# Optimization experiments

Hardware: AMD Instinct MI355X
Metric: run time of the kernel (lower is better)

## Reference

```python
import jax, jax.numpy as jnp
import numpy as np
import math

B, L, D, H = 4, 1024, 768, 12
HD = D // H            # 64
MAX_LEN = 1024         # max_sequence_length


def setup_inputs() -> dict:
    key = jax.random.key(0)
    ks = jax.random.split(key, 10)
    s = 0.02
    return {
        "hidden_states": jax.random.normal(ks[0], (B, L, D), dtype=jnp.float32),
        "Wq": jax.random.normal(ks[1], (D, D), dtype=jnp.float32) * s,
        "bq": jnp.zeros((D,), dtype=jnp.float32),
        "Wk": jax.random.normal(ks[2], (D, D), dtype=jnp.float32) * s,
        "bk": jnp.zeros((D,), dtype=jnp.float32),
        "Wv": jax.random.normal(ks[3], (D, D), dtype=jnp.float32) * s,
        "bv": jnp.zeros((D,), dtype=jnp.float32),
        "Wd": jax.random.normal(ks[4], (D, D), dtype=jnp.float32) * s,
        "bd": jnp.zeros((D,), dtype=jnp.float32),
        "dist_emb": jax.random.normal(ks[5], (2 * MAX_LEN - 1, HD), dtype=jnp.float32) * s,
    }


def reference(hidden_states, Wq, bq, Wk, bk, Wv, bv, Wd, bd, dist_emb):
    b, l, d = hidden_states.shape
    h, hd = H, HD

    def split_heads(x):  # [b,l,d] -> [b,h,l,hd]
        return x.reshape(b, l, h, hd).transpose(0, 2, 1, 3)

    q = split_heads(hidden_states @ Wq + bq)
    k = split_heads(hidden_states @ Wk + bk)
    v = split_heads(hidden_states @ Wv + bv)

    # content-content scores
    scores = jnp.einsum('bhld,bhrd->bhlr', q, k)

    # relative position embedding lookup: distance in [-(l-1), l-1] shifted by MAX_LEN-1
    dist = jnp.arange(l)[:, None] - jnp.arange(l)[None, :] + (MAX_LEN - 1)
    pos = dist_emb[dist].astype(q.dtype)  # [l, l, hd]

    rel_q = jnp.einsum('bhld,lrd->bhlr', q, pos)
    rel_k = jnp.einsum('bhrd,lrd->bhlr', k, pos)
    scores = (scores + rel_q + rel_k) / math.sqrt(hd)

    probs = jax.nn.softmax(scores, axis=-1)  # dropout p=0 (eval)
    ctx = jnp.einsum('bhlr,bhrd->bhld', probs, v)
    ctx = ctx.transpose(0, 2, 1, 3).reshape(b, l, d)
    return ctx @ Wd + bd
```

## Files before the change

### kernel.cpp

```cpp
#include <hip/hip_runtime.h>
#include <hip/hip_bf16.h>
#include <math.h>

typedef __bf16 bf16x8 __attribute__((ext_vector_type(8)));
typedef float f32x4 __attribute__((ext_vector_type(4)));

#define AS1 __attribute__((address_space(1)))
#define AS3 __attribute__((address_space(3)))
typedef AS1 const void gvoid;
typedef AS3 void svoid;

namespace {
constexpr int Bc = 4, Lc = 1024, Dc = 768, Hc = 12, HDc = 64;
constexpr int NKT = 24;
}

static __device__ __forceinline__ ushort f2bf(float f) {
    __hip_bfloat16 h = __float2bfloat16(f);
    return *reinterpret_cast<ushort*>(&h);
}
static __device__ __forceinline__ float bf2f(ushort u) {
    __hip_bfloat16 h;
    *reinterpret_cast<ushort*>(&h) = u;
    return __bfloat162float(h);
}

static __device__ __forceinline__ int sw_us(int row, int col) {
    int line = row >> 1;
    int slot = (((row & 1) << 2) + (col >> 3)) ^ (line & 7);
    return line * 64 + slot * 8 + (col & 7);
}

static __device__ __forceinline__ int o64(int row, int col) {
    return (row << 6) + ((((col >> 3) ^ (row & 7))) << 3) + (col & 7);
}

__global__ void cvt_bf16_k(const float* __restrict__ in, ushort* __restrict__ out,
                           int n, int ntot) {
    int i = blockIdx.x * 256 + threadIdx.x;
    if (i < ntot) out[i] = (i < n) ? f2bf(in[i]) : (ushort)0;
}

__global__ __launch_bounds__(256) void prep_hs(const float* __restrict__ hs,
                                               ushort* __restrict__ oh) {
    int i = blockIdx.x * 256 + threadIdx.x;
    int m = i / 96, c8 = i % 96;
    const float* src = hs + (size_t)m * Dc + c8 * 8;
    float4 x0 = *(const float4*)src;
    float4 x1 = *(const float4*)(src + 4);
    float xs[8] = {x0.x, x0.y, x0.z, x0.w, x1.x, x1.y, x1.z, x1.w};
    ushort hi[8];
#pragma unroll
    for (int j = 0; j < 8; ++j) hi[j] = f2bf(xs[j]);
    int col = c8 * 8, kt = col >> 5, kc = col & 31;
    int mt = m >> 7, row = m & 127;
    int off = (mt * NKT + kt) * 4096 + sw_us(row, kc);
    *(uint4*)(oh + off) = *(uint4*)hi;
}

__global__ __launch_bounds__(256) void prep_w(
    const float* __restrict__ Wq, const float* __restrict__ Wk,
    const float* __restrict__ Wv, const float* __restrict__ Wd,
    ushort* __restrict__ qkvh,
    ushort* __restrict__ wdh, ushort* __restrict__ wdl) {
    int i = blockIdx.x * 256 + threadIdx.x;
    int k = i / 384, n8 = i % 384;
    int which = n8 / 96, nl = (n8 % 96) * 8;
    const float* W = which == 0 ? Wq : which == 1 ? Wk : which == 2 ? Wv : Wd;
    const float* src = W + (size_t)k * Dc + nl;
    float4 x0 = *(const float4*)src;
    float4 x1 = *(const float4*)(src + 4);
    float xs[8] = {x0.x, x0.y, x0.z, x0.w, x1.x, x1.y, x1.z, x1.w};
    int kt = k >> 5, kc = k & 31;
    ushort* dh = (which < 3) ? qkvh : wdh;
    int ngbase = (which < 3) ? which * Dc + nl : nl;
#pragma unroll
    for (int j = 0; j < 8; ++j) {
        float x = xs[j];
        ushort hi = f2bf(x);
        int ng = ngbase + j;
        int nt = ng >> 7, row = ng & 127;
        int off = (nt * NKT + kt) * 4096 + sw_us(row, kc);
        dh[off] = hi;
        if (which == 3) wdl[off] = f2bf(x - bf2f(hi));
    }
}

__global__ __launch_bounds__(256) void gemm_qkv(
    const ushort* __restrict__ Ah, const ushort* __restrict__ Bh,
    const float* __restrict__ b0, const float* __restrict__ b1,
    const float* __restrict__ b2,
    ushort* __restrict__ o0, ushort* __restrict__ o1, ushort* __restrict__ o2) {
    __shared__ uint4 lds4[2][512];

    const int nt = blockIdx.x, mt = blockIdx.y;
    const int tid = threadIdx.x, w = tid >> 6, lane = tid & 63;
    const int wr = w >> 1, wc = w & 1, r = lane & 15, g = lane >> 4;

    const ushort* gsrc = ((w < 2) ? Ah + (size_t)mt * NKT * 4096
                                  : Bh + (size_t)nt * NKT * 4096) + (w & 1) * 2048;
    ushort* ldst = (ushort*)&lds4[w >> 1][0] + (w & 1) * 2048;

    f32x4 acc[4][4];
#pragma unroll
    for (int a = 0; a < 4; ++a)
#pragma unroll
        for (int b = 0; b < 4; ++b) acc[a][b] = (f32x4){0.f, 0.f, 0.f, 0.f};

    for (int kt = 0; kt < NKT; ++kt) {
        __syncthreads();
        const ushort* s = gsrc + kt * 4096 + lane * 8;
#pragma unroll
        for (int c = 0; c < 4; ++c)
            __builtin_amdgcn_global_load_lds((gvoid*)(s + c * 512),
                                             (svoid*)(ldst + c * 512), 16, 0, 0);
        __syncthreads();

        bf16x8 af[4];
#pragma unroll
        for (int mf = 0; mf < 4; ++mf)
            af[mf] = *(const bf16x8*)((const ushort*)&lds4[0][0] +
                                      sw_us(wr * 64 + mf * 16 + r, g * 8));
#pragma unroll
        for (int nf = 0; nf < 4; ++nf) {
            bf16x8 bf = *(const bf16x8*)((const ushort*)&lds4[1][0] +
                                         sw_us(wc * 64 + nf * 16 + r, g * 8));
#pragma unroll
            for (int mf = 0; mf < 4; ++mf)
                acc[mf][nf] = __builtin_amdgcn_mfma_f32_16x16x32_bf16(af[mf], bf, acc[mf][nf], 0, 0, 0);
        }
    }

    const int which = nt / 6;
    const float* bias = which == 0 ? b0 : which == 1 ? b1 : b2;
    ushort* outp = which == 0 ? o0 : which == 1 ? o1 : o2;
    const int nbase = nt * 128 - which * Dc + wc * 64;
    if (which < 2) {
#pragma unroll
        for (int nf = 0; nf < 4; ++nf) {
            int nl = nbase + nf * 16 + r;
            float bb = bias[nl];
            int h = nl >> 6, d = nl & 63;
#pragma unroll
            for (int mf = 0; mf < 4; ++mf) {
                int mbase = mt * 128 + wr * 64 + mf * 16 + g * 4;
#pragma unroll
                for (int i = 0; i < 4; ++i) {
                    int m = mbase + i, bI = m >> 10, l = m & 1023;
                    outp[(((size_t)bI * Hc + h) * Lc + l) * HDc + d] =
                        f2bf(acc[mf][nf][i] + bb);
                }
            }
        }
    } else {
#pragma unroll
        for (int nf = 0; nf < 4; ++nf) {
            int nl = nbase + nf * 16 + r;
            float bb = bias[nl];
            int h = nl >> 6, d = nl & 63;
#pragma unroll
            for (int mf = 0; mf < 4; ++mf) {
                int mbase = mt * 128 + wr * 64 + mf * 16 + g * 4;
                int bI = mbase >> 10, l = mbase & 1023;
                ushort4 c;
                c.x = f2bf(acc[mf][nf][0] + bb);
                c.y = f2bf(acc[mf][nf][1] + bb);
                c.z = f2bf(acc[mf][nf][2] + bb);
                c.w = f2bf(acc[mf][nf][3] + bb);
                *(ushort4*)&outp[((size_t)(bI * Hc + h) * HDc + d) * Lc + l] = c;
            }
        }
    }
}

__global__ __launch_bounds__(256) void gemm_split(
    const ushort* __restrict__ Ah, const ushort* __restrict__ Al,
    const ushort* __restrict__ Bh, const ushort* __restrict__ Bl,
    const float* __restrict__ b0,
    float* __restrict__ of) {
    __shared__ uint4 lds4[4][512];

    const int nt = blockIdx.x, mt = blockIdx.y;
    const int tid = threadIdx.x, w = tid >> 6, lane = tid & 63;
    const int wr = w >> 1, wc = w & 1, r = lane & 15, g = lane >> 4;

    const ushort* gsrc;
    if (w == 0)      gsrc = Ah + (size_t)mt * NKT * 4096;
    else if (w == 1) gsrc = Al + (size_t)mt * NKT * 4096;
    else if (w == 2) gsrc = Bh + (size_t)nt * NKT * 4096;
    else             gsrc = Bl + (size_t)nt * NKT * 4096;
    ushort* ldst = (ushort*)&lds4[w][0];

    f32x4 acc[4][4];
#pragma unroll
    for (int a = 0; a < 4; ++a)
#pragma unroll
        for (int b = 0; b < 4; ++b) acc[a][b] = (f32x4){0.f, 0.f, 0.f, 0.f};

    for (int kt = 0; kt < NKT; ++kt) {
        __syncthreads();
        const ushort* s = gsrc + kt * 4096 + lane * 8;
#pragma unroll
        for (int c = 0; c < 8; ++c)
            __builtin_amdgcn_global_load_lds((gvoid*)(s + c * 512),
                                             (svoid*)(ldst + c * 512), 16, 0, 0);
        __syncthreads();

        bf16x8 af[4][2];
#pragma unroll
        for (int mf = 0; mf < 4; ++mf) {
            int off = sw_us(wr * 64 + mf * 16 + r, g * 8);
            af[mf][0] = *(const bf16x8*)((const ushort*)&lds4[0][0] + off);
            af[mf][1] = *(const bf16x8*)((const ushort*)&lds4[1][0] + off);
        }
#pragma unroll
        for (int nf = 0; nf < 4; ++nf) {
            int off = sw_us(wc * 64 + nf * 16 + r, g * 8);
            bf16x8 bh = *(const bf16x8*)((const ushort*)&lds4[2][0] + off);
            bf16x8 bl = *(const bf16x8*)((const ushort*)&lds4[3][0] + off);
#pragma unroll
            for (int mf = 0; mf < 4; ++mf) {
                acc[mf][nf] = __builtin_amdgcn_mfma_f32_16x16x32_bf16(af[mf][0], bh, acc[mf][nf], 0, 0, 0);
                acc[mf][nf] = __builtin_amdgcn_mfma_f32_16x16x32_bf16(af[mf][0], bl, acc[mf][nf], 0, 0, 0);
                acc[mf][nf] = __builtin_amdgcn_mfma_f32_16x16x32_bf16(af[mf][1], bh, acc[mf][nf], 0, 0, 0);
            }
        }
    }

#pragma unroll
    for (int nf = 0; nf < 4; ++nf) {
        int n = nt * 128 + wc * 64 + nf * 16 + r;
        float bb = b0[n];
#pragma unroll
        for (int mf = 0; mf < 4; ++mf) {
            int mbase = mt * 128 + wr * 64 + mf * 16 + g * 4;
#pragma unroll
            for (int i = 0; i < 4; ++i) {
                int m = mbase + i;
                of[(size_t)m * Dc + n] = acc[mf][nf][i] + bb;
            }
        }
    }
}

__global__ __launch_bounds__(256, 3) void attn_mfma(
    const ushort* __restrict__ qg, const ushort* __restrict__ kg,
    const ushort* __restrict__ vtg, const ushort* __restrict__ Eb,
    ushort* __restrict__ ctxh, ushort* __restrict__ ctxl)
{
    const int b = blockIdx.z, h = blockIdx.y;
    const int l0 = blockIdx.x * 64;
    const size_t bh = (size_t)(b * Hc + h) * Lc * HDc;
    const ushort* qh = qg + bh;
    const ushort* kh = kg + bh;
    const ushort* vth = vtg + bh;

    __shared__ ushort sK[64 * 64];
    __shared__ ushort sVt[64 * 64];
    __shared__ ushort sE[128 * 64];
    __shared__ ushort sQE[64 * 70];
    __shared__ ushort sKE[64 * 70];

    const int tid = threadIdx.x;
    const int lane = tid & 63;
    const int w = tid >> 6;
    const int g = lane >> 4;
    const int r = lane & 15;

    bf16x8 qf0, qf1;
    {
        const ushort* qrow = qh + (size_t)(l0 + 16 * w + r) * 64;
        qf0 = *reinterpret_cast<const bf16x8*>(qrow + g * 8);
        qf1 = *reinterpret_cast<const bf16x8*>(qrow + 32 + g * 8);
    }

    f32x4 cacc[4];
#pragma unroll
    for (int cf = 0; cf < 4; ++cf) cacc[cf] = (f32x4){0.f, 0.f, 0.f, 0.f};
    float mrun[4], lrun[4];
#pragma unroll
    for (int i = 0; i < 4; ++i) { mrun[i] = -1e30f; lrun[i] = 0.f; }

    for (int r0 = 0; r0 < Lc; r0 += 64) {
        __syncthreads();
#pragma unroll
        for (int i = 0; i < 2; ++i) {
            int idx = tid + i * 256;
            int row = idx >> 3, seg = idx & 7;
            int d = (row << 6) + ((seg ^ (row & 7)) << 3);
            *reinterpret_cast<uint4*>(&sK[d]) =
                *reinterpret_cast<const uint4*>(kh + (size_t)(r0 + row) * 64 + seg * 8);
            *reinterpret_cast<uint4*>(&sVt[d]) =
                *reinterpret_cast<const uint4*>(vth + (size_t)row * Lc + r0 + seg * 8);
        }
        const int jb = l0 - r0 + 960;
#pragma unroll
        for (int c = tid; c < 1024; c += 256) {
            int row = c >> 3, seg = c & 7;
            uint4 val;
            if (row < 127)
                val = *reinterpret_cast<const uint4*>(Eb + (size_t)(jb + row) * 64 + seg * 8);
            else
                val = make_uint4(0, 0, 0, 0);
            *reinterpret_cast<uint4*>(&sE[(row << 6) + ((seg ^ (row & 7)) << 3)]) = val;
        }
        __syncthreads();

        __builtin_amdgcn_s_setprio(1);
        f32x4 S[4];
#pragma unroll
        for (int cf = 0; cf < 4; ++cf) {
            f32x4 acc = (f32x4){0.f, 0.f, 0.f, 0.f};
            bf16x8 kf0 = *reinterpret_cast<const bf16x8*>(&sK[o64(16 * cf + r, g * 8)]);
            bf16x8 kf1 = *reinterpret_cast<const bf16x8*>(&sK[o64(16 * cf + r, 32 + g * 8)]);
            acc = __builtin_amdgcn_mfma_f32_16x16x32_bf16(qf0, kf0, acc, 0, 0, 0);
            acc = __builtin_amdgcn_mfma_f32_16x16x32_bf16(qf1, kf1, acc, 0, 0, 0);
            S[cf] = acc;
        }
        bf16x8 kaf0 = *reinterpret_cast<const bf16x8*>(&sK[o64(16 * w + r, g * 8)]);
        bf16x8 kaf1 = *reinterpret_cast<const bf16x8*>(&sK[o64(16 * w + r, 32 + g * 8)]);
#pragma unroll
        for (int cc = 0; cc < 5; ++cc) {
            {
                int er = 16 * (w + cc) + r;
                bf16x8 e0 = *reinterpret_cast<const bf16x8*>(&sE[o64(er, g * 8)]);
                bf16x8 e1 = *reinterpret_cast<const bf16x8*>(&sE[o64(er, 32 + g * 8)]);
                f32x4 aq = (f32x4){0.f, 0.f, 0.f, 0.f};
                aq = __builtin_amdgcn_mfma_f32_16x16x32_bf16(qf0, e0, aq, 0, 0, 0);
                aq = __builtin_amdgcn_mfma_f32_16x16x32_bf16(qf1, e1, aq, 0, 0, 0);
#pragma unroll
                for (int i = 0; i < 4; ++i) {
                    int lc = 16 * cc + r - 4 * g - i;
                    if ((unsigned)lc < 64u)
                        sQE[(16 * w + 4 * g + i) * 70 + lc] = f2bf(aq[i]);
                }
            }
            {
                int er = 16 * (3 - w + cc) + r;
                bf16x8 e0 = *reinterpret_cast<const bf16x8*>(&sE[o64(er, g * 8)]);
                bf16x8 e1 = *reinterpret_cast<const bf16x8*>(&sE[o64(er, 32 + g * 8)]);
                f32x4 ak = (f32x4){0.f, 0.f, 0.f, 0.f};
                ak = __builtin_amdgcn_mfma_f32_16x16x32_bf16(kaf0, e0, ak, 0, 0, 0);
                ak = __builtin_amdgcn_mfma_f32_16x16x32_bf16(kaf1, e1, ak, 0, 0, 0);
#pragma unroll
                for (int i = 0; i < 4; ++i) {
                    int lc = 16 * cc + r + 4 * g + i - 15;
                    if ((unsigned)lc < 64u)
                        sKE[(16 * w + 4 * g + i) * 70 + lc] = f2bf(ak[i]);
                }
            }
        }
        __builtin_amdgcn_s_setprio(0);
        __syncthreads();

        float p[4][4];
#pragma unroll
        for (int cf = 0; cf < 4; ++cf) {
#pragma unroll
            for (int i = 0; i < 4; ++i) {
                int qr = 16 * w + 4 * g + i;
                int kc = 16 * cf + r;
                p[cf][i] = (S[cf][i] + bf2f(sQE[qr * 70 + 63 - kc])
                                     + bf2f(sKE[kc * 70 + qr])) * 0.125f;
            }
        }
#pragma unroll
        for (int i = 0; i < 4; ++i) {
            float m0 = fmaxf(fmaxf(p[0][i], p[1][i]), fmaxf(p[2][i], p[3][i]));
#pragma unroll
            for (int off = 1; off < 16; off <<= 1) m0 = fmaxf(m0, __shfl_xor(m0, off));
            float mn = fmaxf(mrun[i], m0);
            float sc = __expf(mrun[i] - mn);
            mrun[i] = mn;
            float rsum = 0.f;
#pragma unroll
            for (int cf = 0; cf < 4; ++cf) {
                float e = __expf(p[cf][i] - mn);
                p[cf][i] = e;
                rsum += e;
            }
#pragma unroll
            for (int off = 1; off < 16; off <<= 1) rsum += __shfl_xor(rsum, off);
            lrun[i] = lrun[i] * sc + rsum;
#pragma unroll
            for (int cf = 0; cf < 4; ++cf) cacc[cf][i] *= sc;
        }
#pragma unroll
        for (int cf = 0; cf < 4; ++cf)
#pragma unroll
            for (int i = 0; i < 4; ++i)
                sE[o64(16 * w + 4 * g + i, 16 * cf + r)] = f2bf(p[cf][i]);
        __syncthreads();

        __builtin_amdgcn_s_setprio(1);
        bf16x8 pf0 = *reinterpret_cast<const bf16x8*>(&sE[o64(16 * w + r, g * 8)]);
        bf16x8 pf1 = *reinterpret_cast<const bf16x8*>(&sE[o64(16 * w + r, 32 + g * 8)]);
#pragma unroll
        for (int cf = 0; cf < 4; ++cf) {
            bf16x8 vf0 = *reinterpret_cast<const bf16x8*>(&sVt[o64(16 * cf + r, g * 8)]);
            bf16x8 vf1 = *reinterpret_cast<const bf16x8*>(&sVt[o64(16 * cf + r, 32 + g * 8)]);
            cacc[cf] = __builtin_amdgcn_mfma_f32_16x16x32_bf16(pf0, vf0, cacc[cf], 0, 0, 0);
            cacc[cf] = __builtin_amdgcn_mfma_f32_16x16x32_bf16(pf1, vf1, cacc[cf], 0, 0, 0);
        }
        __builtin_amdgcn_s_setprio(0);
    }

    float rinv[4];
#pragma unroll
    for (int i = 0; i < 4; ++i) rinv[i] = 1.0f / lrun[i];
#pragma unroll
    for (int cf = 0; cf < 4; ++cf) {
#pragma unroll
        for (int i = 0; i < 4; ++i) {
            int qr = 16 * w + 4 * g + i;
            float val = cacc[cf][i] * rinv[i];
            ushort hi = f2bf(val);
            ushort lo = f2bf(val - bf2f(hi));
            int m = b * Lc + l0 + qr;
            int c = h * HDc + 16 * cf + r;
            int off = ((m >> 7) * NKT + (c >> 5)) * 4096 + sw_us(m & 127, c & 31);
            ctxh[off] = hi;
            ctxl[off] = lo;
        }
    }
}

extern "C" void kernel_launch(void* const* d_in, const int* in_sizes, int n_in,
                              void* d_out, int out_size, void* d_ws, size_t ws_size,
                              hipStream_t stream) {
    const float* hs = (const float*)d_in[0];
    const float* Wq = (const float*)d_in[1];
    const float* bq = (const float*)d_in[2];
    const float* Wk = (const float*)d_in[3];
    const float* bk = (const float*)d_in[4];
    const float* Wv = (const float*)d_in[5];
    const float* bv = (const float*)d_in[6];
    const float* Wd = (const float*)d_in[7];
    const float* bd = (const float*)d_in[8];
    const float* Eg = (const float*)d_in[9];

    const size_t N = (size_t)Bc * Lc * Dc;
    ushort* p = (ushort*)d_ws;
    ushort* qbf   = p;               p += N;
    ushort* kbf   = p;               p += N;
    ushort* vbf   = p;               p += N;
    ushort* hsh   = p;               p += N;
    ushort* hsl   = p;               p += N;
    ushort* wqkvh = p;               p += (size_t)2304 * 768;
    ushort* Ebf   = p;               p += (size_t)2048 * HDc;
    ushort* wdh   = p;               p += (size_t)768 * 768;
    ushort* wdl   = p;               p += (size_t)768 * 768;

    const int NE = (2 * 1024 - 1) * HDc;
    const int NEP = 2048 * HDc;

    cvt_bf16_k<<<dim3(512), dim3(256), 0, stream>>>(Eg, Ebf, NE, NEP);
    prep_hs<<<dim3(1536), dim3(256), 0, stream>>>(hs, hsh);
    prep_w<<<dim3(1152), dim3(256), 0, stream>>>(Wq, Wk, Wv, Wd, wqkvh, wdh, wdl);

    gemm_qkv<<<dim3(18, 32), dim3(256), 0, stream>>>(
        hsh, wqkvh, bq, bk, bv, qbf, kbf, vbf);

    attn_mfma<<<dim3(16, Hc, Bc), dim3(256), 0, stream>>>(
        qbf, kbf, vbf, Ebf, hsh, hsl);

    gemm_split<<<dim3(6, 32), dim3(256), 0, stream>>>(
        hsh, hsl, wdh, wdl, bd, (float*)d_out);
}
```

Before: 251.3 us.

## Prefetch attention tiles into registers and halve output GEMM N-tile

The attention loop now issues global loads for the next K, V^T and distance-embedding tiles into registers before computing the current tile, overlapping memory latency with MFMA work. It also removes a barrier after writing probabilities to shared memory, relying on each wave touching only its own rows. The output projection GEMM uses 64-wide N tiles, doubling the block count to improve occupancy across CUs. In exchange, the attention kernel needs more registers, and the missing barrier is a correctness risk.

```diff
diff --git a/kernel.cpp b/kernel.cpp
--- a/kernel.cpp
+++ b/kernel.cpp
@@ -178,46 +178,56 @@
     const ushort* __restrict__ Bh, const ushort* __restrict__ Bl,
     const float* __restrict__ b0,
     float* __restrict__ of) {
-    __shared__ uint4 lds4[4][512];
-
-    const int nt = blockIdx.x, mt = blockIdx.y;
+    __shared__ ushort sA[2][4096];
+    __shared__ ushort sB[2][2048];
+
+    const int nt = blockIdx.x;
+    const int mt = blockIdx.y;
     const int tid = threadIdx.x, w = tid >> 6, lane = tid & 63;
     const int wr = w >> 1, wc = w & 1, r = lane & 15, g = lane >> 4;
-
-    const ushort* gsrc;
-    if (w == 0)      gsrc = Ah + (size_t)mt * NKT * 4096;
-    else if (w == 1) gsrc = Al + (size_t)mt * NKT * 4096;
-    else if (w == 2) gsrc = Bh + (size_t)nt * NKT * 4096;
-    else             gsrc = Bl + (size_t)nt * NKT * 4096;
-    ushort* ldst = (ushort*)&lds4[w][0];
-
-    f32x4 acc[4][4];
+    const int nt2 = nt >> 1, nhalf = nt & 1;
+
+    const ushort* srcs[6];
+    ushort* dsts[6];
+#pragma unroll
+    for (int j = 0; j < 6; ++j) {
+        int c = 6 * w + j;
+        if (c < 8)       { srcs[j] = Ah + (size_t)mt * NKT * 4096 + c * 512;
+                           dsts[j] = &sA[0][0] + c * 512; }
+        else if (c < 16) { srcs[j] = Al + (size_t)mt * NKT * 4096 + (c - 8) * 512;
+                           dsts[j] = &sA[1][0] + (c - 8) * 512; }
+        else if (c < 20) { srcs[j] = Bh + (size_t)nt2 * NKT * 4096 + nhalf * 2048 + (c - 16) * 512;
+                           dsts[j] = &sB[0][0] + (c - 16) * 512; }
+        else             { srcs[j] = Bl + (size_t)nt2 * NKT * 4096 + nhalf * 2048 + (c - 20) * 512;
+                           dsts[j] = &sB[1][0] + (c - 20) * 512; }
+    }
+
+    f32x4 acc[4][2];
 #pragma unroll
     for (int a = 0; a < 4; ++a)
 #pragma unroll
-        for (int b = 0; b < 4; ++b) acc[a][b] = (f32x4){0.f, 0.f, 0.f, 0.f};
+        for (int b = 0; b < 2; ++b) acc[a][b] = (f32x4){0.f, 0.f, 0.f, 0.f};
 
     for (int kt = 0; kt < NKT; ++kt) {
         __syncthreads();
-        const ushort* s = gsrc + kt * 4096 + lane * 8;
-#pragma unroll
-        for (int c = 0; c < 8; ++c)
-            __builtin_amdgcn_global_load_lds((gvoid*)(s + c * 512),
-                                             (svoid*)(ldst + c * 512), 16, 0, 0);
+#pragma unroll
+        for (int j = 0; j < 6; ++j)
+            __builtin_amdgcn_global_load_lds((gvoid*)(srcs[j] + (size_t)kt * 4096 + lane * 8),
+                                             (svoid*)(dsts[j]), 16, 0, 0);
         __syncthreads();
 
         bf16x8 af[4][2];
 #pragma unroll
         for (int mf = 0; mf < 4; ++mf) {
             int off = sw_us(wr * 64 + mf * 16 + r, g * 8);
-            af[mf][0] = *(const bf16x8*)((const ushort*)&lds4[0][0] + off);
-            af[mf][1] = *(const bf16x8*)((const ushort*)&lds4[1][0] + off);
-        }
-#pragma unroll
-        for (int nf = 0; nf < 4; ++nf) {
-            int off = sw_us(wc * 64 + nf * 16 + r, g * 8);
-            bf16x8 bh = *(const bf16x8*)((const ushort*)&lds4[2][0] + off);
-            bf16x8 bl = *(const bf16x8*)((const ushort*)&lds4[3][0] + off);
+            af[mf][0] = *(const bf16x8*)(&sA[0][0] + off);
+            af[mf][1] = *(const bf16x8*)(&sA[1][0] + off);
+        }
+#pragma unroll
+        for (int nf = 0; nf < 2; ++nf) {
+            int off = sw_us(nhalf * 64 + wc * 32 + nf * 16 + r, g * 8) - nhalf * 2048;
+            bf16x8 bh = *(const bf16x8*)(&sB[0][0] + off);
+            bf16x8 bl = *(const bf16x8*)(&sB[1][0] + off);
 #pragma unroll
             for (int mf = 0; mf < 4; ++mf) {
                 acc[mf][nf] = __builtin_amdgcn_mfma_f32_16x16x32_bf16(af[mf][0], bh, acc[mf][nf], 0, 0, 0);
@@ -228,8 +238,8 @@
     }
 
 #pragma unroll
-    for (int nf = 0; nf < 4; ++nf) {
-        int n = nt * 128 + wc * 64 + nf * 16 + r;
+    for (int nf = 0; nf < 2; ++nf) {
+        int n = nt * 64 + wc * 32 + nf * 16 + r;
         float bb = b0[n];
 #pragma unroll
         for (int mf = 0; mf < 4; ++mf) {
@@ -267,6 +277,9 @@
     const int g = lane >> 4;
     const int r = lane & 15;
 
+    const int rowA = tid >> 3;
+    const int segA = tid & 7;
+
     bf16x8 qf0, qf1;
     {
         const ushort* qrow = qh + (size_t)(l0 + 16 * w + r) * 64;
@@ -274,6 +287,20 @@
         qf1 = *reinterpret_cast<const bf16x8*>(qrow + 32 + g * 8);
     }
 
+    uint4 rK0, rK1, rV0, rV1, rE0, rE1, rE2, rE3;
+    auto ISSUE = [&](int r0) {
+        rK0 = *(const uint4*)(kh + (size_t)(r0 + rowA) * 64 + segA * 8);
+        rK1 = *(const uint4*)(kh + (size_t)(r0 + rowA + 32) * 64 + segA * 8);
+        rV0 = *(const uint4*)(vth + (size_t)rowA * Lc + r0 + segA * 8);
+        rV1 = *(const uint4*)(vth + (size_t)(rowA + 32) * Lc + r0 + segA * 8);
+        int jb = l0 - r0 + 960;
+        rE0 = *(const uint4*)(Eb + (size_t)(jb + rowA) * 64 + segA * 8);
+        rE1 = *(const uint4*)(Eb + (size_t)(jb + rowA + 32) * 64 + segA * 8);
+        rE2 = *(const uint4*)(Eb + (size_t)(jb + rowA + 64) * 64 + segA * 8);
+        rE3 = *(const uint4*)(Eb + (size_t)(jb + rowA + 96) * 64 + segA * 8);
+    };
+    ISSUE(0);
+
     f32x4 cacc[4];
 #pragma unroll
     for (int cf = 0; cf < 4; ++cf) cacc[cf] = (f32x4){0.f, 0.f, 0.f, 0.f};
@@ -283,27 +310,17 @@
 
     for (int r0 = 0; r0 < Lc; r0 += 64) {
         __syncthreads();
-#pragma unroll
-        for (int i = 0; i < 2; ++i) {
-            int idx = tid + i * 256;
-            int row = idx >> 3, seg = idx & 7;
-            int d = (row << 6) + ((seg ^ (row & 7)) << 3);
-            *reinterpret_cast<uint4*>(&sK[d]) =
-                *reinterpret_cast<const uint4*>(kh + (size_t)(r0 + row) * 64 + seg * 8);
-            *reinterpret_cast<uint4*>(&sVt[d]) =
-                *reinterpret_cast<const uint4*>(vth + (size_t)row * Lc + r0 + seg * 8);
-        }
-        const int jb = l0 - r0 + 960;
-#pragma unroll
-        for (int c = tid; c < 1024; c += 256) {
-            int row = c >> 3, seg = c & 7;
-            uint4 val;
-            if (row < 127)
-                val = *reinterpret_cast<const uint4*>(Eb + (size_t)(jb + row) * 64 + seg * 8);
-            else
-                val = make_uint4(0, 0, 0, 0);
-            *reinterpret_cast<uint4*>(&sE[(row << 6) + ((seg ^ (row & 7)) << 3)]) = val;
-        }
+        {
+            int d0 = (rowA << 6) + ((segA ^ (rowA & 7)) << 3);
+            int d1 = d0 + 32 * 64;
+            *(uint4*)&sK[d0] = rK0;  *(uint4*)&sK[d1] = rK1;
+            *(uint4*)&sVt[d0] = rV0; *(uint4*)&sVt[d1] = rV1;
+            *(uint4*)&sE[d0] = rE0;
+            *(uint4*)&sE[d0 + 32 * 64] = rE1;
+            *(uint4*)&sE[d0 + 64 * 64] = rE2;
+            *(uint4*)&sE[d0 + 96 * 64] = rE3;
+        }
+        if (r0 + 64 < Lc) ISSUE(r0 + 64);
         __syncthreads();
 
         __builtin_amdgcn_s_setprio(1);
@@ -390,7 +407,6 @@
 #pragma unroll
             for (int i = 0; i < 4; ++i)
                 sE[o64(16 * w + 4 * g + i, 16 * cf + r)] = f2bf(p[cf][i]);
-        __syncthreads();
 
         __builtin_amdgcn_s_setprio(1);
         bf16x8 pf0 = *reinterpret_cast<const bf16x8*>(&sE[o64(16 * w + r, g * 8)]);
@@ -464,6 +480,6 @@
     attn_mfma<<<dim3(16, Hc, Bc), dim3(256), 0, stream>>>(
         qbf, kbf, vbf, Ebf, hsh, hsl);
 
-    gemm_split<<<dim3(6, 32), dim3(256), 0, stream>>>(
+    gemm_split<<<dim3(12, 32), dim3(256), 0, stream>>>(
         hsh, hsl, wdh, wdl, bd, (float*)d_out);
 }
```

After: 245.3 us. 2.4% less time.
